# Performance work log

Hardware: AMD Instinct MI355X
Metric: run time of the kernel (lower is better)

Reference implementation:

```python
import jax, jax.numpy as jnp
import numpy as np

V = 131072          # total vertices (hits) across all events
K = 64              # neighbours per vertex, col 0 == self
NSEG = 4            # number of events (row splits segments)
THRESHOLD = 0.5     # hierarchy score cut (layer's non-trainable threshold var)


def setup_inputs() -> dict:
    key = jax.random.key(0)
    k1, k2 = jax.random.split(key)
    score = jax.random.uniform(k1, (V, 1), dtype=jnp.float32)
    seg = V // NSEG
    base = (jnp.arange(V, dtype=jnp.int32) // seg) * seg
    # random neighbours constrained to the same segment; column 0 is self
    rnd = jax.random.randint(k2, (V, K - 1), 0, seg, dtype=jnp.int32) + base[:, None]
    nidxs = jnp.concatenate([jnp.arange(V, dtype=jnp.int32)[:, None], rnd], axis=1)
    row_splits = (jnp.arange(NSEG + 1, dtype=jnp.int32) * seg)
    return {"score": score, "nidxs": nidxs, "row_splits": row_splits}


def _local_group(score1, nidxs, row_splits, thr):
    """Greedy threshold-based neighbour grouping (HGCalML LocalGroup op).

    Vertices are visited per segment in descending score order. An unused
    vertex becomes a group seed; if its score > thr it absorbs all of its
    not-yet-used neighbours. Returns fixed-shape (-1 padded) outputs so the
    whole thing is jit-compatible.
    """
    V_, K_ = nidxs.shape
    seg_id = jnp.searchsorted(row_splits, jnp.arange(V_, dtype=row_splits.dtype),
                              side='right') - 1
    # per-segment descending-score order == tf.argsort(DESC) per row split
    order = jnp.lexsort((-score1, seg_id)).astype(jnp.int32)
    kcols = jnp.arange(K_)

    def step(state, v):
        used, assign, dirn, sel, seed, count = state
        is_new = jnp.logical_not(used[v])                 # v not grouped yet -> seed
        expand = score1[v] > thr                          # absorb neighbours?
        cand = jnp.where(expand, nidxs[v],
                         jnp.where(kcols == 0, v, -1))    # else only self
        safe = jnp.clip(cand, 0, V_ - 1)
        valid = (cand >= 0) & jnp.logical_not(used[safe]) & is_new
        used = used.at[safe].set(used[safe] | valid)
        assign = assign.at[safe].set(jnp.where(valid, count, assign[safe]))
        dirn = dirn.at[v].set(jnp.where(valid, cand, -1))
        sel = sel.at[count].set(jnp.where(is_new, v, sel[count]))
        seed = seed.at[v].set(seed[v] | is_new)
        count = count + is_new.astype(jnp.int32)
        return (used, assign, dirn, sel, seed, count), None

    init = (jnp.zeros(V_, dtype=bool),                 # used
            jnp.full(V_, -1, jnp.int32),               # backgather: seed rank per vertex
            jnp.full((V_, K_), -1, jnp.int32),         # directed neighbour idxs
            jnp.full(V_, -1, jnp.int32),               # selected seed vertices, -1 padded
            jnp.zeros(V_, dtype=bool),                 # seed mask
            jnp.int32(0))
    (used, assign, dirn, sel, seed, count), _ = jax.lax.scan(step, init, order)
    cs0 = jnp.concatenate([jnp.zeros(1, jnp.int32),
                           jnp.cumsum(seed.astype(jnp.int32))])
    rs_new = cs0[row_splits]                           # new row splits over seeds
    return rs_new, dirn, sel[:, None], assign, count


def reference(score, nidxs, row_splits):
    # layer: score = clip(score, 0, 1); per-segment argsort; LocalGroup
    score1 = jnp.clip(score.reshape(-1), 0.0, 1.0)
    rs_new, dirnidx, sel, backgather, n_sel = _local_group(score1, nidxs,
                                                           row_splits, THRESHOLD)
    # return_backscatter=True -> back = [V, sel]; we return sel (padded) + n_sel
    # outputs: directed nidx (V,K), selection idxs (V,1 padded with -1),
    #          backgather (V,), new row splits, number selected
    return dirnidx, sel, backgather, rs_new, n_sel
```

## Files before the change

### kernel.cpp

```cpp
#include <hip/hip_runtime.h>
#include <stdint.h>

#define INFU 0xFFFFFFFFu
#define LCAP 24576
#define NC 128

__global__ void __launch_bounds__(256) k_hist(const float* score, unsigned* bcnt,
                                              unsigned* claim, int* sel, int V, int SEGN){
  int v = blockIdx.x*blockDim.x+threadIdx.x; if (v>=V) return;
  claim[v]=INFU;
  sel[v]=-1;
  float s = score[v]; s = fminf(fmaxf(s,0.f),1.f);
  int b = (int)(s*(float)SEGN); if (b>=SEGN) b=SEGN-1; if (b<0) b=0;
  int bd = SEGN-1-b;
  int seg = v / SEGN;
  atomicAdd(&bcnt[(size_t)seg*SEGN+bd], 1u);
}

__global__ void __launch_bounds__(1024) k_scan(const unsigned* in, const unsigned* claim,
                                               unsigned* outExcl, unsigned* segTotal,
                                               int SEGN, int mode){
  int seg = blockIdx.x; int tid = threadIdx.x; int lane = tid&63, wv = tid>>6;
  __shared__ unsigned wsum[16];
  const int CH = (SEGN+1023)>>10;
  int i0 = tid*CH, i1 = i0+CH; if (i1>SEGN) i1=SEGN;
  const size_t base = (size_t)seg*SEGN;
  unsigned sum=0;
  for (int i=i0;i<i1;i++){
    unsigned x = (mode==0)? in[base+i] : ((claim[base+i]==INFU)?1u:0u);
    sum+=x;
  }
  unsigned incl=sum;
  for (int off=1;off<64;off<<=1){ unsigned t=__shfl_up(incl,(unsigned)off); if (lane>=off) incl+=t; }
  if (lane==63) wsum[wv]=incl;
  __syncthreads();
  unsigned wbase=0,total=0;
  for (int w=0;w<16;w++){ unsigned s=wsum[w]; if (w<wv) wbase+=s; total+=s; }
  unsigned run = wbase + incl - sum;
  for (int i=i0;i<i1;i++){
    unsigned x = (mode==0)? in[base+i] : ((claim[base+i]==INFU)?1u:0u);
    outExcl[base+i]=run; run+=x;
  }
  if (tid==0 && segTotal) segTotal[seg]=total;
}

__global__ void __launch_bounds__(256) k_scatter(const float* score, const unsigned* bbase,
                                                 unsigned* bfill, unsigned long long* slot,
                                                 int V, int SEGN){
  int v = blockIdx.x*blockDim.x+threadIdx.x; if (v>=V) return;
  float s = score[v]; s=fminf(fmaxf(s,0.f),1.f);
  int b=(int)(s*(float)SEGN); if(b>=SEGN)b=SEGN-1; if(b<0)b=0;
  int bd=SEGN-1-b; int seg=v/SEGN;
  size_t bk = (size_t)seg*SEGN+bd;
  unsigned pos = bbase[bk] + atomicAdd(&bfill[bk],1u);
  unsigned kb = ~__float_as_uint(s);
  slot[(size_t)seg*SEGN+pos] = ((unsigned long long)kb<<32) | (unsigned)v;
}

__global__ void __launch_bounds__(256) k_bsort(const unsigned* bcnt, const unsigned* bbase,
                                               unsigned long long* slot, int V, int SEGN){
  int t = blockIdx.x*blockDim.x+threadIdx.x; if (t>=V) return;
  unsigned n = bcnt[t];
  if (n<2) return;
  int seg = t / SEGN;
  unsigned long long* a = slot + (size_t)seg*SEGN + bbase[t];
  for (unsigned i=1;i<n;i++){
    unsigned long long key=a[i]; int j=(int)i-1;
    while (j>=0 && a[j]>key){ a[j+1]=a[j]; j--; }
    a[j+1]=key;
  }
}

__global__ void __launch_bounds__(256) k_build(const unsigned long long* slot,
                                               int* ord, unsigned* rnkv, int* segE,
                                               int V, int SEGN){
  int r = blockIdx.x*blockDim.x+threadIdx.x; if (r>=V) return;
  unsigned long long sl = slot[r];
  int v = (int)(unsigned)(sl & 0xFFFFFFFFull);
  ord[r]=v;
  int seg = r / SEGN; int rl = r - seg*SEGN;
  rnkv[v] = (unsigned)rl;
  float s = __uint_as_float(~(unsigned)(sl>>32));
  bool ex = (s > 0.5f);
  if (rl==0 && !ex) segE[seg]=0;
  if (ex){
    if (rl==SEGN-1) segE[seg]=SEGN;
    else {
      float s2 = __uint_as_float(~(unsigned)(slot[r+1]>>32));
      if (!(s2 > 0.5f)) segE[seg]=rl+1;
    }
  }
}

__global__ void __launch_bounds__(256) k_pack4(const int* ord, const unsigned* rnkv, const int* nidxs,
                                               const int* segE, unsigned short* nbr16,
                                               int V, int K, int SEGN){
  const int K4 = K>>2;
  long long q = (long long)blockIdx.x*256 + threadIdx.x;
  if (q >= (long long)V*K4) return;
  int gr = (int)(q / K4); int k4 = (int)(q - (long long)gr*K4);
  int seg = gr / SEGN, r = gr - seg*SEGN;
  if (r >= segE[seg]) return;
  int v = ord[gr];
  const int4 nn = *(const int4*)(nidxs + (size_t)v*K + (size_t)k4*4);
  ushort4 o;
  o.x=(unsigned short)rnkv[nn.x]; o.y=(unsigned short)rnkv[nn.y];
  o.z=(unsigned short)rnkv[nn.z]; o.w=(unsigned short)rnkv[nn.w];
  *(ushort4*)(nbr16 + (size_t)gr*K + (size_t)k4*4) = o;
}
__global__ void __launch_bounds__(256) k_pack(const int* ord, const unsigned* rnkv, const int* nidxs,
                                              const int* segE, unsigned short* nbr16,
                                              int V, int K, int SEGN){
  long long t = (long long)blockIdx.x*256 + threadIdx.x;
  if (t >= (long long)V*K) return;
  int gr = (int)(t / K); int k = (int)(t - (long long)gr*K);
  int seg = gr / SEGN, r = gr - seg*SEGN;
  if (r >= segE[seg]) return;
  int v = ord[gr];
  int w = nidxs[(size_t)v*K + k];
  nbr16[t] = (unsigned short)rnkv[w];
}

__global__ void __launch_bounds__(1024) k_greedy(const unsigned short* nbr16, const int* segE,
                                                 unsigned* claim, int SEGN, int K){
  __shared__ unsigned s_cl[LCAP/2];
  __shared__ unsigned char s_pos[LCAP];
  __shared__ unsigned s_cand[NC];
  __shared__ unsigned long long s_McLo[NC];
  __shared__ unsigned long long s_McHi[NC];
  __shared__ unsigned long long s_anyLo, s_anyHi;
  __shared__ unsigned long long s_bm[16];
  __shared__ unsigned s_wcur;
  __shared__ unsigned long long s_v0, s_v1;
  const int seg = blockIdx.x, tid = threadIdx.x, lane = tid&63, wv = tid>>6;
  unsigned* clg = claim + (size_t)seg*SEGN;
  const int E = segE[seg];
  const int cap = (LCAP < SEGN) ? LCAP : SEGN;
  const int capw = (cap+1)>>1;
  for (int i=tid; i<capw; i+=1024) s_cl[i]=0xFFFFFFFFu;
  for (int i=tid; i<((cap+3)>>2); i+=1024) ((unsigned*)s_pos)[i]=0u;
  if (tid<NC) s_cand[tid]=INFU;
  const unsigned long long lt_mask = (lane==0) ? 0ull : ((~0ull) >> (64-lane));
  unsigned wcursor = 0;
  for (;;){
    __syncthreads();
    if (tid<NC){
      unsigned pc = s_cand[tid];
      if (pc!=INFU && pc<(unsigned)cap) s_pos[pc]=0;
      s_cand[tid]=INFU; s_McLo[tid]=0ull; s_McHi[tid]=0ull;
    }
    if (tid==NC)   s_anyLo=0ull;
    if (tid==NC+1) s_anyHi=0ull;
    int found = 0;
    for (;;){
      unsigned r = wcursor + (unsigned)(wv*64 + lane);
      bool undec=false;
      if (r<(unsigned)E){
        if (r<(unsigned)cap)
          undec = (((s_cl[r>>1]>>((r&1)*16))&0xFFFFu)==0xFFFFu);
        else
          undec = (__hip_atomic_load(&clg[r], __ATOMIC_RELAXED, __HIP_MEMORY_SCOPE_AGENT)==INFU);
      }
      unsigned long long m = __ballot(undec);
      if (lane==0) s_bm[wv]=m;
      __syncthreads();
      unsigned long long mb = (lane<16)? s_bm[lane] : 0ull;
      int pc16 = (int)__popcll(mb);
      int incl = pc16;
      #pragma unroll
      for (int off=1; off<16; off<<=1){ int t=__shfl_up(incl,off); if (lane>=off) incl+=t; }
      int total = __shfl(incl, 15);
      int below = __shfl(incl, wv) - __shfl(pc16, wv);
      int pos = found + below + (int)__popcll(m & lt_mask);
      if (undec && pos<NC){
        s_cand[pos]=r;
        if (r<(unsigned)cap) s_pos[r]=(unsigned char)(pos+1);
      }
      if (undec && pos==NC-1) s_wcur=r+1;
      bool filled = (found+total>=NC);
      bool winend = (wcursor + 1024 >= (unsigned)E);
      __syncthreads();
      if (filled){ wcursor = s_wcur; found=NC; break; }
      found += total;
      if (winend){ wcursor=(unsigned)E; break; }
      wcursor += 1024;
    }
    const int ncand = found;
    if (!ncand) break;
    unsigned rwq[8], cq[8];
    #pragma unroll
    for (int q=0;q<8;q++){
      int c=(wv<<3)|q;
      cq[q] = (c<ncand) ? s_cand[c] : INFU;
    }
    #pragma unroll
    for (int q=0;q<8;q++){
      rwq[q]=INFU;
      if (cq[q]!=INFU && lane<K)
        rwq[q] = (unsigned)nbr16[((size_t)seg*SEGN + cq[q])*K + lane];
    }
    const bool fastmap = (s_cand[ncand-1] < (unsigned)cap);
    #pragma unroll
    for (int q=0;q<8;q++){
      int c=(wv<<3)|q;
      if (cq[q]!=INFU){
        unsigned rw = rwq[q];
        int p = -1;
        if (fastmap){
          if (rw<(unsigned)cap){ p = (int)s_pos[rw] - 1; }
        } else {
          int pp=0;
          if (s_cand[pp+64]<=rw) pp+=64;
          if (s_cand[pp+32]<=rw) pp+=32;
          if (s_cand[pp+16]<=rw) pp+=16;
          if (s_cand[pp+8 ]<=rw) pp+=8;
          if (s_cand[pp+4 ]<=rw) pp+=4;
          if (s_cand[pp+2 ]<=rw) pp+=2;
          if (s_cand[pp+1 ]<=rw) pp+=1;
          if (pp<ncand && s_cand[pp]==rw) p=pp;
        }
        if (lane<K && p>c){
          if (p<64){ atomicOr(&s_McLo[c], 1ull<<p);      atomicOr(&s_anyLo, 1ull<<p); }
          else     { atomicOr(&s_McHi[c], 1ull<<(p-64)); atomicOr(&s_anyHi, 1ull<<(p-64)); }
        }
      }
    }
    __syncthreads();
    if (wv==0){
      const int n0 = (ncand<64)? ncand : 64;
      const int n1 = ncand - n0;
      const unsigned long long nmask0 = (n0==64)? ~0ull : ((1ull<<n0)-1ull);
      unsigned long long Mj0 = s_McLo[lane];
      unsigned long long any0 = s_anyLo & nmask0;
      unsigned long long valid0 = (~any0) & nmask0;
      unsigned long long rem = any0;
      while (rem){
        int i=__builtin_ctzll(rem); rem &= rem-1;
        bool pred = ((valid0>>lane)&1ull) && (lane<i) && ((Mj0>>i)&1ull);
        if (__ballot(pred)==0ull) valid0 |= (1ull<<i);
      }
      unsigned long long valid1 = 0ull;
      if (n1>0){
        const unsigned long long nmask1 = (n1==64)? ~0ull : ((1ull<<n1)-1ull);
        unsigned long long sp = ((valid0>>lane)&1ull) ? s_McHi[lane] : 0ull;
        #pragma unroll
        for (int off=32; off; off>>=1)
          sp |= (unsigned long long)__shfl_xor((long long)sp, off);
        unsigned long long Mj1 = s_McHi[64+lane];
        unsigned long long any1 = s_anyHi & nmask1;
        valid1 = (~(any1|sp)) & nmask1;
        unsigned long long rem1 = any1 & ~sp;
        while (rem1){
          int i=__builtin_ctzll(rem1); rem1 &= rem1-1;
          bool pred = ((valid1>>lane)&1ull) && (lane<i) && ((Mj1>>i)&1ull);
          if (__ballot(pred)==0ull) valid1 |= (1ull<<i);
        }
      }
      if (lane==0){ s_v0=valid0; s_v1=valid1; }
    }
    __syncthreads();
    const unsigned long long v0 = s_v0, v1 = s_v1;
    #pragma unroll
    for (int q=0;q<8;q++){
      int c=(wv<<3)|q;
      bool isv = (c<64) ? (((v0>>c)&1ull)!=0ull) : (((v1>>(c-64))&1ull)!=0ull);
      if (cq[q]!=INFU && isv){
        unsigned rw=rwq[q], cr=cq[q];
        if (rw>cr && rw<(unsigned)E){
          if (rw<(unsigned)cap){
            unsigned idx=rw>>1, sh=(rw&1)*16;
            unsigned old=s_cl[idx];
            for(;;){
              unsigned curv=(old>>sh)&0xFFFFu;
              if (cr>=curv) break;
              unsigned neu=(old & ~(0xFFFFu<<sh)) | (cr<<sh);
              unsigned prev=atomicCAS(&s_cl[idx], old, neu);
              if (prev==old) break;
              old=prev;
            }
          } else {
            atomicMin(&clg[rw], cr);
          }
        }
      }
    }
  }
  __syncthreads();
  for (int r=tid; r<cap; r+=1024){
    unsigned c=(s_cl[r>>1]>>((r&1)*16))&0xFFFFu;
    clg[r] = (c==0xFFFFu) ? INFU : c;
  }
}

__global__ void __launch_bounds__(256) k_commit4(const unsigned short* nbr16, const int* segE,
                                                 unsigned* claim, int V, int K, int SEGN){
  const int K4 = K>>2;
  long long q = (long long)blockIdx.x*256 + threadIdx.x;
  if (q >= (long long)V*K4) return;
  int gr = (int)(q / K4); int k4 = (int)(q - (long long)gr*K4);
  int seg = gr / SEGN; unsigned r = (unsigned)(gr - seg*SEGN);
  if ((int)r >= segE[seg]) return;
  if (claim[gr] != INFU) return;
  ushort4 nb = *(const ushort4*)(nbr16 + (size_t)gr*K + (size_t)k4*4);
  unsigned* cl = claim + (size_t)seg*SEGN;
  if ((unsigned)nb.x > r) atomicMin(&cl[nb.x], r);
  if ((unsigned)nb.y > r) atomicMin(&cl[nb.y], r);
  if ((unsigned)nb.z > r) atomicMin(&cl[nb.z], r);
  if ((unsigned)nb.w > r) atomicMin(&cl[nb.w], r);
}
__global__ void __launch_bounds__(256) k_commit(const unsigned short* nbr16, const int* segE,
                                                unsigned* claim, int V, int K, int SEGN){
  long long t = (long long)blockIdx.x*256 + threadIdx.x;
  if (t >= (long long)V*K) return;
  int gr = (int)(t / K);
  int seg = gr / SEGN, r = gr - seg*SEGN;
  if (r >= segE[seg]) return;
  if (claim[gr] != INFU) return;
  unsigned rw = nbr16[t];
  if (rw > (unsigned)r) atomicMin(&claim[(size_t)seg*SEGN + rw], (unsigned)r);
}

__global__ void __launch_bounds__(256) k_dirnAll4(const int* nidxs, const unsigned* rnkv,
                                                  const unsigned* claim, const float* score,
                                                  const unsigned* segTotal,
                                                  const unsigned* srank,
                                                  int* dirn, int* sel, int* backg,
                                                  int* rs, int* nsel,
                                                  int V, int K, int SEGN, int NSEG){
  const int K4 = K>>2;
  long long q = (long long)blockIdx.x*256 + threadIdx.x;
  if (q >= (long long)V*K4) return;
  int v = (int)(q / K4); int k4 = (int)(q - (long long)v*K4);
  int seg = v / SEGN;
  if (q <= (long long)NSEG){
    unsigned run=0;
    for (int s=0;s<(int)q;s++) run+=segTotal[s];
    rs[q]=(int)run;
    if ((int)q==NSEG) nsel[0]=(int)run;
  }
  const unsigned* cl = claim + (size_t)seg*SEGN;
  unsigned r = rnkv[v];
  unsigned c = cl[r];
  if (k4==0){
    unsigned segOff=0;
    for (int s=0;s<seg;s++) segOff+=segTotal[s];
    unsigned a = (c==INFU)? r : c;
    unsigned g = segOff + srank[(size_t)seg*SEGN + a];
    backg[v] = (int)g;
    if (c==INFU) sel[g] = v;
  }
  int4 o = make_int4(-1,-1,-1,-1);
  if (c == INFU){
    float s = score[v]; s=fminf(fmaxf(s,0.f),1.f);
    if (!(s > 0.5f)){
      if (k4==0) o.x = v;
    } else {
      const int4 nn = *(const int4*)(nidxs + (size_t)v*K + (size_t)k4*4);
      unsigned rw, cw, aw;
      rw=rnkv[nn.x]; cw=cl[rw]; aw=(cw==INFU)?rw:cw; if (aw==r) o.x=nn.x;
      rw=rnkv[nn.y]; cw=cl[rw]; aw=(cw==INFU)?rw:cw; if (aw==r) o.y=nn.y;
      rw=rnkv[nn.z]; cw=cl[rw]; aw=(cw==INFU)?rw:cw; if (aw==r) o.z=nn.z;
      rw=rnkv[nn.w]; cw=cl[rw]; aw=(cw==INFU)?rw:cw; if (aw==r) o.w=nn.w;
    }
  }
  *(int4*)(dirn + (size_t)v*K + (size_t)k4*4) = o;
}
__global__ void __launch_bounds__(256) k_dirnAll(const int* nidxs, const unsigned* rnkv,
                                                 const unsigned* claim, const float* score,
                                                 const unsigned* segTotal,
                                                 const unsigned* srank,
                                                 int* dirn, int* sel, int* backg,
                                                 int* rs, int* nsel,
                                                 int V, int K, int SEGN, int NSEG){
  long long t = (long long)blockIdx.x*blockDim.x + threadIdx.x;
  if (t >= (long long)V*K) return;
  int v = (int)(t / K); int j = (int)(t - (long long)v*K);
  int seg = v / SEGN;
  if (t <= (long long)NSEG){
    unsigned run=0;
    for (int s=0;s<(int)t;s++) run+=segTotal[s];
    rs[t]=(int)run;
    if ((int)t==NSEG) nsel[0]=(int)run;
  }
  const unsigned* cl = claim + (size_t)seg*SEGN;
  unsigned r = rnkv[v];
  unsigned c = cl[r];
  if (j==0){
    unsigned segOff=0;
    for (int s=0;s<seg;s++) segOff+=segTotal[s];
    unsigned a = (c==INFU)? r : c;
    unsigned g = segOff + srank[(size_t)seg*SEGN + a];
    backg[v] = (int)g;
    if (c==INFU) sel[g] = v;
  }
  int out;
  if (c != INFU){
    out = -1;
  } else {
    float s = score[v]; s=fminf(fmaxf(s,0.f),1.f);
    if (!(s > 0.5f)){
      out = (j==0)? v : -1;
    } else {
      int w = nidxs[(size_t)v*K + j];
      unsigned rw = rnkv[w];
      unsigned cw = cl[rw];
      unsigned aw = (cw==INFU)? rw : cw;
      out = (aw == r)? w : -1;
    }
  }
  dirn[t] = out;
}

extern "C" void kernel_launch(void* const* d_in, const int* in_sizes, int n_in,
                              void* d_out, int out_size, void* d_ws, size_t ws_size,
                              hipStream_t stream) {
  const float* score   = (const float*)d_in[0];
  const int*   nidxs   = (const int*)d_in[1];
  (void)d_in[2];

  const int V    = in_sizes[0];
  const int K    = in_sizes[1] / V;
  const int NSEG = in_sizes[2] - 1;
  const int SEGN = V / NSEG;

  char* w = (char*)d_ws;
  unsigned long long* slot = (unsigned long long*)w;  w += (size_t)V*8;
  unsigned* bcnt  = (unsigned*)w; w += (size_t)V*4;
  unsigned* bfill = (unsigned*)w; w += (size_t)V*4;
  unsigned* bbase = (unsigned*)w; w += (size_t)V*4;
  int*      ord   = (int*)w;      w += (size_t)V*4;
  unsigned* rnkv  = (unsigned*)w; w += (size_t)V*4;
  unsigned* claim = (unsigned*)w; w += (size_t)V*4;
  unsigned* srank = (unsigned*)w; w += (size_t)V*4;
  unsigned* segTotal = (unsigned*)w; w += 64;
  int*      segE     = (int*)w;      w += 64;

  int* out      = (int*)d_out;
  int* out_dirn = out;
  int* out_sel  = out + (size_t)V*K;
  int* out_bg   = out_sel + V;
  int* out_rs   = out_bg + V;
  int* out_nsel = out_rs + (NSEG+1);

  unsigned short* nbr16 = (unsigned short*)out_dirn;

  hipMemsetAsync(bcnt,  0x00, (size_t)V*8, stream);

  int nb256 = (V + 255)/256;
  long long totVK = (long long)V*K;
  int nbVK = (int)((totVK + 255)/256);
  const bool vec4 = (K>=4) && ((K&3)==0);
  int nbQ = (int)(((long long)V*(K>>2) + 255)/256);

  k_hist<<<nb256, 256, 0, stream>>>(score, bcnt, claim, out_sel, V, SEGN);
  k_scan<<<NSEG, 1024, 0, stream>>>(bcnt, nullptr, bbase, nullptr, SEGN, 0);
  k_scatter<<<nb256, 256, 0, stream>>>(score, bbase, bfill, slot, V, SEGN);
  k_bsort<<<nb256, 256, 0, stream>>>(bcnt, bbase, slot, V, SEGN);
  k_build<<<nb256, 256, 0, stream>>>(slot, ord, rnkv, segE, V, SEGN);
  if (vec4) k_pack4<<<nbQ, 256, 0, stream>>>(ord, rnkv, nidxs, segE, nbr16, V, K, SEGN);
  else      k_pack <<<nbVK, 256, 0, stream>>>(ord, rnkv, nidxs, segE, nbr16, V, K, SEGN);
  k_greedy<<<NSEG, 1024, 0, stream>>>(nbr16, segE, claim, SEGN, K);
  if (vec4) k_commit4<<<nbQ, 256, 0, stream>>>(nbr16, segE, claim, V, K, SEGN);
  else      k_commit <<<nbVK, 256, 0, stream>>>(nbr16, segE, claim, V, K, SEGN);
  k_scan<<<NSEG, 1024, 0, stream>>>(nullptr, claim, srank, segTotal, SEGN, 1);
  if (vec4) k_dirnAll4<<<nbQ, 256, 0, stream>>>(nidxs, rnkv, claim, score, segTotal, srank,
                                                out_dirn, out_sel, out_bg, out_rs, out_nsel,
                                                V, K, SEGN, NSEG);
  else      k_dirnAll<<<nbVK, 256, 0, stream>>>(nidxs, rnkv, claim, score, segTotal, srank,
                                                out_dirn, out_sel, out_bg, out_rs, out_nsel,
                                                V, K, SEGN, NSEG);
}
```

Baseline: 383.5 us.

## Double greedy candidate batch to 256 with four-word conflict bitmasks

Each round of the per-segment greedy kernel now resolves 256 candidate seeds instead of 128. This halves the number of serialized rounds and block-wide barriers. The conflict matrix and the sequential validity resolution are generalized from two 64-bit words to four, carrying suppression across word blocks. s_pos is widened to 16 bits, and the shared-memory claim cache shrinks to make room. The trade-offs are more conflicts per batch, longer serial ballot loops in wave 0, more registers per thread, and a smaller LDS-resident region, so more claims fall back to global atomics.

```diff
diff --git a/kernel.cpp b/kernel.cpp
--- a/kernel.cpp
+++ b/kernel.cpp
@@ -2,8 +2,8 @@
 #include <stdint.h>
 
 #define INFU 0xFFFFFFFFu
-#define LCAP 24576
-#define NC 128
+#define LCAP 20480
+#define NC 256
 
 __global__ void __launch_bounds__(256) k_hist(const float* score, unsigned* bcnt,
                                               unsigned* claim, int* sel, int V, int SEGN){
@@ -124,21 +124,20 @@
 __global__ void __launch_bounds__(1024) k_greedy(const unsigned short* nbr16, const int* segE,
                                                  unsigned* claim, int SEGN, int K){
   __shared__ unsigned s_cl[LCAP/2];
-  __shared__ unsigned char s_pos[LCAP];
+  __shared__ unsigned short s_pos[LCAP];
   __shared__ unsigned s_cand[NC];
-  __shared__ unsigned long long s_McLo[NC];
-  __shared__ unsigned long long s_McHi[NC];
-  __shared__ unsigned long long s_anyLo, s_anyHi;
+  __shared__ unsigned long long s_McW[4][NC];
+  __shared__ unsigned long long s_any[4];
   __shared__ unsigned long long s_bm[16];
   __shared__ unsigned s_wcur;
-  __shared__ unsigned long long s_v0, s_v1;
+  __shared__ unsigned long long s_v[4];
   const int seg = blockIdx.x, tid = threadIdx.x, lane = tid&63, wv = tid>>6;
   unsigned* clg = claim + (size_t)seg*SEGN;
   const int E = segE[seg];
   const int cap = (LCAP < SEGN) ? LCAP : SEGN;
   const int capw = (cap+1)>>1;
   for (int i=tid; i<capw; i+=1024) s_cl[i]=0xFFFFFFFFu;
-  for (int i=tid; i<((cap+3)>>2); i+=1024) ((unsigned*)s_pos)[i]=0u;
+  for (int i=tid; i<capw; i+=1024) ((unsigned*)s_pos)[i]=0u;
   if (tid<NC) s_cand[tid]=INFU;
   const unsigned long long lt_mask = (lane==0) ? 0ull : ((~0ull) >> (64-lane));
   unsigned wcursor = 0;
@@ -147,10 +146,10 @@
     if (tid<NC){
       unsigned pc = s_cand[tid];
       if (pc!=INFU && pc<(unsigned)cap) s_pos[pc]=0;
-      s_cand[tid]=INFU; s_McLo[tid]=0ull; s_McHi[tid]=0ull;
-    }
-    if (tid==NC)   s_anyLo=0ull;
-    if (tid==NC+1) s_anyHi=0ull;
+      s_cand[tid]=INFU;
+      s_McW[0][tid]=0ull; s_McW[1][tid]=0ull; s_McW[2][tid]=0ull; s_McW[3][tid]=0ull;
+    }
+    if (tid>=NC && tid<NC+4) s_any[tid-NC]=0ull;
     int found = 0;
     for (;;){
       unsigned r = wcursor + (unsigned)(wv*64 + lane);
@@ -174,7 +173,7 @@
       int pos = found + below + (int)__popcll(m & lt_mask);
       if (undec && pos<NC){
         s_cand[pos]=r;
-        if (r<(unsigned)cap) s_pos[r]=(unsigned char)(pos+1);
+        if (r<(unsigned)cap) s_pos[r]=(unsigned short)(pos+1);
       }
       if (undec && pos==NC-1) s_wcur=r+1;
       bool filled = (found+total>=NC);
@@ -187,22 +186,22 @@
     }
     const int ncand = found;
     if (!ncand) break;
-    unsigned rwq[8], cq[8];
+    unsigned rwq[16], cq[16];
     #pragma unroll
-    for (int q=0;q<8;q++){
-      int c=(wv<<3)|q;
+    for (int q=0;q<16;q++){
+      int c=(wv<<4)|q;
       cq[q] = (c<ncand) ? s_cand[c] : INFU;
     }
     #pragma unroll
-    for (int q=0;q<8;q++){
+    for (int q=0;q<16;q++){
       rwq[q]=INFU;
       if (cq[q]!=INFU && lane<K)
         rwq[q] = (unsigned)nbr16[((size_t)seg*SEGN + cq[q])*K + lane];
     }
     const bool fastmap = (s_cand[ncand-1] < (unsigned)cap);
     #pragma unroll
-    for (int q=0;q<8;q++){
-      int c=(wv<<3)|q;
+    for (int q=0;q<16;q++){
+      int c=(wv<<4)|q;
       if (cq[q]!=INFU){
         unsigned rw = rwq[q];
         int p = -1;
@@ -210,76 +209,81 @@
           if (rw<(unsigned)cap){ p = (int)s_pos[rw] - 1; }
         } else {
           int pp=0;
-          if (s_cand[pp+64]<=rw) pp+=64;
-          if (s_cand[pp+32]<=rw) pp+=32;
-          if (s_cand[pp+16]<=rw) pp+=16;
-          if (s_cand[pp+8 ]<=rw) pp+=8;
-          if (s_cand[pp+4 ]<=rw) pp+=4;
-          if (s_cand[pp+2 ]<=rw) pp+=2;
-          if (s_cand[pp+1 ]<=rw) pp+=1;
+          if (s_cand[pp+128]<=rw) pp+=128;
+          if (s_cand[pp+64 ]<=rw) pp+=64;
+          if (s_cand[pp+32 ]<=rw) pp+=32;
+          if (s_cand[pp+16 ]<=rw) pp+=16;
+          if (s_cand[pp+8  ]<=rw) pp+=8;
+          if (s_cand[pp+4  ]<=rw) pp+=4;
+          if (s_cand[pp+2  ]<=rw) pp+=2;
+          if (s_cand[pp+1  ]<=rw) pp+=1;
           if (pp<ncand && s_cand[pp]==rw) p=pp;
         }
         if (lane<K && p>c){
-          if (p<64){ atomicOr(&s_McLo[c], 1ull<<p);      atomicOr(&s_anyLo, 1ull<<p); }
-          else     { atomicOr(&s_McHi[c], 1ull<<(p-64)); atomicOr(&s_anyHi, 1ull<<(p-64)); }
+          int w2 = p>>6;
+          atomicOr(&s_McW[w2][c], 1ull<<(p&63));
+          atomicOr(&s_any[w2],    1ull<<(p&63));
         }
       }
     }
     __syncthreads();
     if (wv==0){
-      const int n0 = (ncand<64)? ncand : 64;
-      const int n1 = ncand - n0;
-      const unsigned long long nmask0 = (n0==64)? ~0ull : ((1ull<<n0)-1ull);
-      unsigned long long Mj0 = s_McLo[lane];
-      unsigned long long any0 = s_anyLo & nmask0;
-      unsigned long long valid0 = (~any0) & nmask0;
-      unsigned long long rem = any0;
-      while (rem){
-        int i=__builtin_ctzll(rem); rem &= rem-1;
-        bool pred = ((valid0>>lane)&1ull) && (lane<i) && ((Mj0>>i)&1ull);
-        if (__ballot(pred)==0ull) valid0 |= (1ull<<i);
-      }
-      unsigned long long valid1 = 0ull;
-      if (n1>0){
-        const unsigned long long nmask1 = (n1==64)? ~0ull : ((1ull<<n1)-1ull);
-        unsigned long long sp = ((valid0>>lane)&1ull) ? s_McHi[lane] : 0ull;
-        #pragma unroll
-        for (int off=32; off; off>>=1)
-          sp |= (unsigned long long)__shfl_xor((long long)sp, off);
-        unsigned long long Mj1 = s_McHi[64+lane];
-        unsigned long long any1 = s_anyHi & nmask1;
-        valid1 = (~(any1|sp)) & nmask1;
-        unsigned long long rem1 = any1 & ~sp;
-        while (rem1){
-          int i=__builtin_ctzll(rem1); rem1 &= rem1-1;
-          bool pred = ((valid1>>lane)&1ull) && (lane<i) && ((Mj1>>i)&1ull);
-          if (__ballot(pred)==0ull) valid1 |= (1ull<<i);
+      unsigned long long sp1=0ull, sp2=0ull, sp3=0ull;
+      unsigned long long validB[4] = {0ull,0ull,0ull,0ull};
+      #pragma unroll
+      for (int b=0;b<4;b++){
+        int nb = ncand - (b<<6);
+        if (nb>0){
+          if (nb>64) nb=64;
+          const unsigned long long mask = (nb==64)? ~0ull : ((1ull<<nb)-1ull);
+          unsigned long long sp = (b==0)?0ull : (b==1)?sp1 : (b==2)?sp2 : sp3;
+          unsigned long long Mj = s_McW[b][(b<<6)+lane];
+          unsigned long long any = s_any[b] & mask;
+          unsigned long long valid = (~(any|sp)) & mask;
+          unsigned long long rem = any & ~sp;
+          while (rem){
+            int i=__builtin_ctzll(rem); rem &= rem-1;
+            bool pred = ((valid>>lane)&1ull) && (lane<i) && ((Mj>>i)&1ull);
+            if (__ballot(pred)==0ull) valid |= (1ull<<i);
+          }
+          validB[b]=valid;
+          #pragma unroll
+          for (int t2=b+1;t2<4;t2++){
+            if ((t2<<6) < ncand){
+              unsigned long long c2 = ((valid>>lane)&1ull) ? s_McW[t2][(b<<6)+lane] : 0ull;
+              #pragma unroll
+              for (int off=32; off; off>>=1)
+                c2 |= (unsigned long long)__shfl_xor((long long)c2, off);
+              if (t2==1) sp1|=c2; else if (t2==2) sp2|=c2; else sp3|=c2;
+            }
+          }
         }
       }
-      if (lane==0){ s_v0=valid0; s_v1=valid1; }
+      if (lane==0){ s_v[0]=validB[0]; s_v[1]=validB[1]; s_v[2]=validB[2]; s_v[3]=validB[3]; }
     }
     __syncthreads();
-    const unsigned long long v0 = s_v0, v1 = s_v1;
     #pragma unroll
-    for (int q=0;q<8;q++){
-      int c=(wv<<3)|q;
-      bool isv = (c<64) ? (((v0>>c)&1ull)!=0ull) : (((v1>>(c-64))&1ull)!=0ull);
-      if (cq[q]!=INFU && isv){
-        unsigned rw=rwq[q], cr=cq[q];
-        if (rw>cr && rw<(unsigned)E){
-          if (rw<(unsigned)cap){
-            unsigned idx=rw>>1, sh=(rw&1)*16;
-            unsigned old=s_cl[idx];
-            for(;;){
-              unsigned curv=(old>>sh)&0xFFFFu;
-              if (cr>=curv) break;
-              unsigned neu=(old & ~(0xFFFFu<<sh)) | (cr<<sh);
-              unsigned prev=atomicCAS(&s_cl[idx], old, neu);
-              if (prev==old) break;
-              old=prev;
+    for (int q=0;q<16;q++){
+      int c=(wv<<4)|q;
+      if (cq[q]!=INFU){
+        bool isv = ((s_v[c>>6] >> (c&63)) & 1ull) != 0ull;
+        if (isv){
+          unsigned rw=rwq[q], cr=cq[q];
+          if (rw>cr && rw<(unsigned)E){
+            if (rw<(unsigned)cap){
+              unsigned idx=rw>>1, sh=(rw&1)*16;
+              unsigned old=s_cl[idx];
+              for(;;){
+                unsigned curv=(old>>sh)&0xFFFFu;
+                if (cr>=curv) break;
+                unsigned neu=(old & ~(0xFFFFu<<sh)) | (cr<<sh);
+                unsigned prev=atomicCAS(&s_cl[idx], old, neu);
+                if (prev==old) break;
+                old=prev;
+              }
+            } else {
+              atomicMin(&clg[rw], cr);
             }
-          } else {
-            atomicMin(&clg[rw], cr);
           }
         }
       }
```

Result: slower. 399.5 us (+4.2%).

## Drop commit pass, precompute per-vertex absorb array, prefetch upcoming greedy rows

Applied to the files above, without the earlier changes.

Removes the separate commit kernels by letting the greedy kernel apply claims for neighbours beyond the processed range (the bound check changes from rw<E to rw!=INFU). Adds a small k_absorb kernel that materializes each vertex's owning seed rank, so the dirn kernels need one gather per neighbour instead of a rank lookup followed by a claim lookup. The greedy loop also touches the neighbour rows of upcoming undecided candidates with volatile loads to warm the cache. This adds extra global atomics inside the serial greedy kernel and some wasted prefetch traffic.

```diff
diff --git a/kernel.cpp b/kernel.cpp
--- a/kernel.cpp
+++ b/kernel.cpp
@@ -199,6 +199,20 @@
       if (cq[q]!=INFU && lane<K)
         rwq[q] = (unsigned)nbr16[((size_t)seg*SEGN + cq[q])*K + lane];
     }
+    {
+      unsigned pr = wcursor + (unsigned)(wv*64 + lane);
+      if (pr < (unsigned)E){
+        bool und = (pr<(unsigned)cap)
+                   ? (((s_cl[pr>>1]>>((pr&1)*16))&0xFFFFu)==0xFFFFu)
+                   : (__hip_atomic_load(&clg[pr], __ATOMIC_RELAXED, __HIP_MEMORY_SCOPE_AGENT)==INFU);
+        if (und){
+          const unsigned short* rp = nbr16 + ((size_t)seg*SEGN + pr)*K;
+          unsigned a0 = *(const volatile unsigned short*)rp;
+          unsigned a1 = (K>32)? *(const volatile unsigned short*)(rp+32) : 0u;
+          asm volatile("" :: "v"(a0), "v"(a1));
+        }
+      }
+    }
     const bool fastmap = (s_cand[ncand-1] < (unsigned)cap);
     #pragma unroll
     for (int q=0;q<8;q++){
@@ -266,7 +280,7 @@
       bool isv = (c<64) ? (((v0>>c)&1ull)!=0ull) : (((v1>>(c-64))&1ull)!=0ull);
       if (cq[q]!=INFU && isv){
         unsigned rw=rwq[q], cr=cq[q];
-        if (rw>cr && rw<(unsigned)E){
+        if (rw>cr && rw!=INFU){
           if (rw<(unsigned)cap){
             unsigned idx=rw>>1, sh=(rw&1)*16;
             unsigned old=s_cl[idx];
@@ -292,36 +306,17 @@
   }
 }
 
-__global__ void __launch_bounds__(256) k_commit4(const unsigned short* nbr16, const int* segE,
-                                                 unsigned* claim, int V, int K, int SEGN){
-  const int K4 = K>>2;
-  long long q = (long long)blockIdx.x*256 + threadIdx.x;
-  if (q >= (long long)V*K4) return;
-  int gr = (int)(q / K4); int k4 = (int)(q - (long long)gr*K4);
-  int seg = gr / SEGN; unsigned r = (unsigned)(gr - seg*SEGN);
-  if ((int)r >= segE[seg]) return;
-  if (claim[gr] != INFU) return;
-  ushort4 nb = *(const ushort4*)(nbr16 + (size_t)gr*K + (size_t)k4*4);
-  unsigned* cl = claim + (size_t)seg*SEGN;
-  if ((unsigned)nb.x > r) atomicMin(&cl[nb.x], r);
-  if ((unsigned)nb.y > r) atomicMin(&cl[nb.y], r);
-  if ((unsigned)nb.z > r) atomicMin(&cl[nb.z], r);
-  if ((unsigned)nb.w > r) atomicMin(&cl[nb.w], r);
-}
-__global__ void __launch_bounds__(256) k_commit(const unsigned short* nbr16, const int* segE,
-                                                unsigned* claim, int V, int K, int SEGN){
-  long long t = (long long)blockIdx.x*256 + threadIdx.x;
-  if (t >= (long long)V*K) return;
-  int gr = (int)(t / K);
-  int seg = gr / SEGN, r = gr - seg*SEGN;
-  if (r >= segE[seg]) return;
-  if (claim[gr] != INFU) return;
-  unsigned rw = nbr16[t];
-  if (rw > (unsigned)r) atomicMin(&claim[(size_t)seg*SEGN + rw], (unsigned)r);
+__global__ void __launch_bounds__(256) k_absorb(const unsigned* rnkv, const unsigned* claim,
+                                                unsigned* absorb, int V, int SEGN){
+  int v = blockIdx.x*blockDim.x+threadIdx.x; if (v>=V) return;
+  int seg = v / SEGN;
+  unsigned r = rnkv[v];
+  unsigned c = claim[(size_t)seg*SEGN + r];
+  absorb[v] = (c==INFU)? r : c;
 }
 
 __global__ void __launch_bounds__(256) k_dirnAll4(const int* nidxs, const unsigned* rnkv,
-                                                  const unsigned* claim, const float* score,
+                                                  const unsigned* absorb, const float* score,
                                                   const unsigned* segTotal,
                                                   const unsigned* srank,
                                                   int* dirn, int* sel, int* backg,
@@ -338,35 +333,33 @@
     rs[q]=(int)run;
     if ((int)q==NSEG) nsel[0]=(int)run;
   }
-  const unsigned* cl = claim + (size_t)seg*SEGN;
   unsigned r = rnkv[v];
-  unsigned c = cl[r];
+  unsigned a_self = absorb[v];
+  bool seed = (a_self == r);
   if (k4==0){
     unsigned segOff=0;
     for (int s=0;s<seg;s++) segOff+=segTotal[s];
-    unsigned a = (c==INFU)? r : c;
-    unsigned g = segOff + srank[(size_t)seg*SEGN + a];
+    unsigned g = segOff + srank[(size_t)seg*SEGN + a_self];
     backg[v] = (int)g;
-    if (c==INFU) sel[g] = v;
+    if (seed) sel[g] = v;
   }
   int4 o = make_int4(-1,-1,-1,-1);
-  if (c == INFU){
+  if (seed){
     float s = score[v]; s=fminf(fmaxf(s,0.f),1.f);
     if (!(s > 0.5f)){
       if (k4==0) o.x = v;
     } else {
       const int4 nn = *(const int4*)(nidxs + (size_t)v*K + (size_t)k4*4);
-      unsigned rw, cw, aw;
-      rw=rnkv[nn.x]; cw=cl[rw]; aw=(cw==INFU)?rw:cw; if (aw==r) o.x=nn.x;
-      rw=rnkv[nn.y]; cw=cl[rw]; aw=(cw==INFU)?rw:cw; if (aw==r) o.y=nn.y;
-      rw=rnkv[nn.z]; cw=cl[rw]; aw=(cw==INFU)?rw:cw; if (aw==r) o.z=nn.z;
-      rw=rnkv[nn.w]; cw=cl[rw]; aw=(cw==INFU)?rw:cw; if (aw==r) o.w=nn.w;
+      if (absorb[nn.x]==r) o.x=nn.x;
+      if (absorb[nn.y]==r) o.y=nn.y;
+      if (absorb[nn.z]==r) o.z=nn.z;
+      if (absorb[nn.w]==r) o.w=nn.w;
     }
   }
   *(int4*)(dirn + (size_t)v*K + (size_t)k4*4) = o;
 }
 __global__ void __launch_bounds__(256) k_dirnAll(const int* nidxs, const unsigned* rnkv,
-                                                 const unsigned* claim, const float* score,
+                                                 const unsigned* absorb, const float* score,
                                                  const unsigned* segTotal,
                                                  const unsigned* srank,
                                                  int* dirn, int* sel, int* backg,
@@ -382,30 +375,24 @@
     rs[t]=(int)run;
     if ((int)t==NSEG) nsel[0]=(int)run;
   }
-  const unsigned* cl = claim + (size_t)seg*SEGN;
   unsigned r = rnkv[v];
-  unsigned c = cl[r];
+  unsigned a_self = absorb[v];
+  bool seed = (a_self == r);
   if (j==0){
     unsigned segOff=0;
     for (int s=0;s<seg;s++) segOff+=segTotal[s];
-    unsigned a = (c==INFU)? r : c;
-    unsigned g = segOff + srank[(size_t)seg*SEGN + a];
+    unsigned g = segOff + srank[(size_t)seg*SEGN + a_self];
     backg[v] = (int)g;
-    if (c==INFU) sel[g] = v;
-  }
-  int out;
-  if (c != INFU){
-    out = -1;
-  } else {
+    if (seed) sel[g] = v;
+  }
+  int out = -1;
+  if (seed){
     float s = score[v]; s=fminf(fmaxf(s,0.f),1.f);
     if (!(s > 0.5f)){
       out = (j==0)? v : -1;
     } else {
       int w = nidxs[(size_t)v*K + j];
-      unsigned rw = rnkv[w];
-      unsigned cw = cl[rw];
-      unsigned aw = (cw==INFU)? rw : cw;
-      out = (aw == r)? w : -1;
+      out = (absorb[w] == r)? w : -1;
     }
   }
   dirn[t] = out;
@@ -434,6 +421,7 @@
   unsigned* srank = (unsigned*)w; w += (size_t)V*4;
   unsigned* segTotal = (unsigned*)w; w += 64;
   int*      segE     = (int*)w;      w += 64;
+  unsigned* absorb = bcnt;
 
   int* out      = (int*)d_out;
   int* out_dirn = out;
@@ -460,13 +448,12 @@
   if (vec4) k_pack4<<<nbQ, 256, 0, stream>>>(ord, rnkv, nidxs, segE, nbr16, V, K, SEGN);
   else      k_pack <<<nbVK, 256, 0, stream>>>(ord, rnkv, nidxs, segE, nbr16, V, K, SEGN);
   k_greedy<<<NSEG, 1024, 0, stream>>>(nbr16, segE, claim, SEGN, K);
-  if (vec4) k_commit4<<<nbQ, 256, 0, stream>>>(nbr16, segE, claim, V, K, SEGN);
-  else      k_commit <<<nbVK, 256, 0, stream>>>(nbr16, segE, claim, V, K, SEGN);
   k_scan<<<NSEG, 1024, 0, stream>>>(nullptr, claim, srank, segTotal, SEGN, 1);
-  if (vec4) k_dirnAll4<<<nbQ, 256, 0, stream>>>(nidxs, rnkv, claim, score, segTotal, srank,
+  k_absorb<<<nb256, 256, 0, stream>>>(rnkv, claim, absorb, V, SEGN);
+  if (vec4) k_dirnAll4<<<nbQ, 256, 0, stream>>>(nidxs, rnkv, absorb, score, segTotal, srank,
                                                 out_dirn, out_sel, out_bg, out_rs, out_nsel,
                                                 V, K, SEGN, NSEG);
-  else      k_dirnAll<<<nbVK, 256, 0, stream>>>(nidxs, rnkv, claim, score, segTotal, srank,
+  else      k_dirnAll<<<nbVK, 256, 0, stream>>>(nidxs, rnkv, absorb, score, segTotal, srank,
                                                 out_dirn, out_sel, out_bg, out_rs, out_nsel,
                                                 V, K, SEGN, NSEG);
 }
```

Result: no change. 384.1 us (+0.1%).
